# Performance work log

Hardware: AMD Instinct MI355X
Metric: run time of the kernel (lower is better)

Reference implementation:

```python
import jax, jax.numpy as jnp
import numpy as np

B, N, FH, H, FO = 8, 1024, 128, 8, 64
FIN = 2 * FH  # f_hid * 2
NEG = -1e9
SLOPE = 0.2  # leaky_relu negative slope (GAT default)


def setup_inputs() -> dict:
    key = jax.random.key(0)
    ks = jax.random.split(key, 10)
    x = jax.random.normal(ks[0], (B, FIN), jnp.float32)
    A = jax.random.randint(ks[1], (B, N, N), 0, 2, jnp.int32)  # 0/1 dense adjacency
    mask_zero = jnp.ones((B, N, 1), jnp.float32)  # node validity mask
    p_atten = jax.random.uniform(ks[2], (B, N), jnp.float32)  # unused in forward body
    e_atten = jax.random.uniform(ks[3], (B, N, FIN), jnp.float32)
    Npost = jax.random.normal(ks[4], (N, FIN), jnp.float32) * np.float32(1.0 / np.sqrt(FIN))  # kaiming-ish
    w = jax.random.normal(ks[5], (H, FIN, FO), jnp.float32) * np.float32(1.0 / np.sqrt(FIN))
    a_src = jax.random.normal(ks[6], (H, FO), jnp.float32) * np.float32(0.1)
    a_dst = jax.random.normal(ks[7], (H, FO), jnp.float32) * np.float32(0.1)
    bias = jnp.zeros((FO,), jnp.float32)
    return {"x": x, "A": A, "mask_zero": mask_zero, "p_atten": p_atten,
            "e_atten": e_atten, "Npost": Npost, "w": w, "a_src": a_src,
            "a_dst": a_dst, "bias": bias}


def reference(x, A, mask_zero, p_atten, e_atten, Npost, w, a_src, a_dst, bias):
    # broadcast-mul feature gating: x [B,FIN] repeated over N posts, gated by Npost*e_atten
    recx = x[:, None, :] * (Npost[None, :, :] * e_atten)          # [B,N,FIN]
    # BatchGAT (DeepInf-style multi-head graph attention, dropout disabled / eval mode)
    h = jnp.einsum('bnf,hfo->bhno', recx, w)                      # [B,H,N,FO]
    s = jnp.einsum('bhno,ho->bhn', h, a_src)                      # src attention term
    d = jnp.einsum('bhno,ho->bhn', h, a_dst)                      # dst attention term
    logits = jax.nn.leaky_relu(s[:, :, :, None] + d[:, :, None, :], SLOPE)  # [B,H,N,N]
    adj = (A > 0)[:, None, :, :]                                  # [B,1,N,N]
    logits = jnp.where(adj, logits, NEG)
    attn = jax.nn.softmax(logits, axis=-1)                        # masked row softmax
    out = jnp.einsum('bhnm,bhmo->bhno', attn, h) + bias           # aggregate neighbors
    out = out.mean(axis=1)                                        # average heads -> [B,N,FO]
    return out * mask_zero                                        # zero padded nodes
```

## Files before the change

kernel.cpp:

```cpp
#include <hip/hip_runtime.h>

typedef __attribute__((ext_vector_type(8))) short          bf16x8;
typedef __attribute__((ext_vector_type(8))) unsigned short u16x8;
typedef __attribute__((ext_vector_type(4))) unsigned short u16x4;
typedef __attribute__((ext_vector_type(4))) float          f32x4;
typedef __attribute__((ext_vector_type(4))) unsigned int   u32x4;

union U8 { u16x8 u; bf16x8 b; u32x4 w; };
union U4 { u16x4 u; unsigned w[2]; };

__device__ __forceinline__ unsigned short f2bf(float f){
  unsigned u = __float_as_uint(f);
  return (unsigned short)((u + 0x7fffu + ((u >> 16) & 1u)) >> 16);
}
__device__ __forceinline__ unsigned pack_bf16(float lo, float hi){
  unsigned a = __float_as_uint(hi) + 0x8000u;
  unsigned b = __float_as_uint(lo) + 0x8000u;
  return __builtin_amdgcn_perm(a, b, 0x07060302u);
}
__device__ __forceinline__ unsigned maskpack(float e0, float e1, unsigned m){
  unsigned r;
  asm("v_cvt_pk_bf16_f32 %0, %1, %2" : "=v"(r) : "v"(e0), "v"(e1));
  return r & m;
}

#define NN  1024
#define FIN 256
#define NH  8
#define FO  64

__global__ __launch_bounds__(256) void stage0(
    const float* __restrict__ w, unsigned short* __restrict__ wfrag)
{
  const int tid = blockIdx.x * 256 + threadIdx.x;
  const int lane = tid & 63, ss = (tid >> 6) & 3, kc = (tid >> 8) & 7, h = tid >> 11;
  const int o = 16 * ss + (lane & 15);
  const int f = kc * 32 + (lane >> 4) * 8;
  u16x8 r;
  #pragma unroll
  for (int j = 0; j < 8; j++) r[j] = f2bf(w[(h * FIN + f + j) * FO + o]);
  *(u16x8*)(wfrag + tid * 8) = r;
}

__global__ __launch_bounds__(512, 4) void stageA(
    const float* __restrict__ x, const float* __restrict__ e_at,
    const float* __restrict__ Np, const unsigned short* __restrict__ wfrag,
    const float* __restrict__ a_src, const float* __restrict__ a_dst,
    const int* __restrict__ A, unsigned long long* __restrict__ Abits,
    unsigned short* __restrict__ hT,
    float* __restrict__ Rt, float* __restrict__ expd, float* __restrict__ expd2)
{
  __shared__ unsigned short rex[16 * 264];
  const int t = threadIdx.x;
  const int n0 = blockIdx.x * 16, b = blockIdx.y;

  {
    const int row = t >> 5, f0 = (t & 31) * 8;
    const int nrow = n0 + row;
    const float* ep = e_at + (b * NN + nrow) * FIN + f0;
    const float* qp = Np + nrow * FIN + f0;
    const float* xp = x + b * FIN + f0;
    f32x4 e0 = *(const f32x4*)ep, e1 = *(const f32x4*)(ep + 4);
    f32x4 q0 = *(const f32x4*)qp, q1 = *(const f32x4*)(qp + 4);
    f32x4 x0 = *(const f32x4*)xp, x1 = *(const f32x4*)(xp + 4);
    u16x8 r;
    #pragma unroll
    for (int j = 0; j < 4; j++){
      r[j]     = f2bf(e0[j] * q0[j] * x0[j]);
      r[j + 4] = f2bf(e1[j] * q1[j] * x1[j]);
    }
    *(u16x8*)(rex + row * 264 + f0) = r;
  }
  __syncthreads();

  const int h = t >> 6, lane = t & 63, quad = lane >> 4, l15 = lane & 15;
  const unsigned short* wf = wfrag + h * 16384 + lane * 8;

  f32x4 acc[4] = {};
  #pragma unroll
  for (int kc = 0; kc < 8; kc++){
    U8 a0, bf[4];
    a0.u = *(const u16x8*)(rex + l15 * 264 + kc * 32 + quad * 8);
    #pragma unroll
    for (int ss = 0; ss < 4; ss++) bf[ss].u = *(const u16x8*)(wf + (kc * 4 + ss) * 512);
    #pragma unroll
    for (int ss = 0; ss < 4; ss++)
      acc[ss] = __builtin_amdgcn_mfma_f32_16x16x32_bf16(a0.b, bf[ss].b, acc[ss], 0, 0, 0);
  }

  {
    const int mtile = blockIdx.x >> 1, moff = (blockIdx.x & 1) * 16;
    unsigned short* pan = hT + (size_t)(((b * NH + h) * 32 + mtile) * 64) * 32;
    #pragma unroll
    for (int ss = 0; ss < 4; ss++){
      U4 v;
      v.w[0] = pack_bf16(acc[ss][0], acc[ss][1]);
      v.w[1] = pack_bf16(acc[ss][2], acc[ss][3]);
      *(u16x4*)(pan + (16 * ss + l15) * 32 + moff + quad * 4) = v.u;
    }
  }

  float as4[4], ad4[4];
  #pragma unroll
  for (int ss = 0; ss < 4; ss++){
    as4[ss] = a_src[h * FO + 16 * ss + l15];
    ad4[ss] = a_dst[h * FO + 16 * ss + l15];
  }
  #pragma unroll
  for (int i = 0; i < 4; i++){
    float ps = 0.f, pd = 0.f;
    #pragma unroll
    for (int ss = 0; ss < 4; ss++){ ps += acc[ss][i] * as4[ss]; pd += acc[ss][i] * ad4[ss]; }
    #pragma unroll
    for (int off = 1; off < 16; off <<= 1){
      ps += __shfl_xor(ps, off);
      pd += __shfl_xor(pd, off);
    }
    if (l15 == 0){
      const int idx = (b * NH + h) * NN + n0 + quad * 4 + i;
      Rt[idx]    = __expf(0.8f * ps);
      expd[idx]  = __expf(pd);
      expd2[idx] = __expf(0.2f * pd);
    }
  }

  {
    const int seg = (b * 64 + blockIdx.x) * 16384;
    #pragma unroll 4
    for (int k = 0; k < 32; k++){
      const int i = seg + k * 512 + t;
      unsigned long long m = __ballot(A[i] > 0);
      if ((t & 63) == 0) Abits[i >> 6] = m;
    }
  }
}

__global__ __launch_bounds__(256, 4) void stageB(
    const unsigned* __restrict__ Aw,
    const unsigned short* __restrict__ hT,
    const float* __restrict__ Rt,
    const float* __restrict__ expd, const float* __restrict__ expd2,
    float* __restrict__ hpart)
{
  __shared__ float smem[4288];
  __shared__ __align__(8) unsigned lut[16][2];

  const int fid = blockIdx.x;
  const int b = fid & 7, h = (fid >> 3) & 7, rt = fid >> 6;
  const int n0 = rt * 64;

  const int t = threadIdx.x;
  const int w = t >> 6, lane = t & 63, quad = lane >> 4, l15 = lane & 15;
  const int rw = w & 1, mh = w >> 1;
  const int nb = n0 + rw * 32;

  if (t < 16){
    lut[t][0] = (t & 1 ? 0xFFFFu : 0u) | (t & 2 ? 0xFFFF0000u : 0u);
    lut[t][1] = (t & 4 ? 0xFFFFu : 0u) | (t & 8 ? 0xFFFF0000u : 0u);
  }
  {
    const float* s1 = expd  + (b * NH + h) * NN;
    const float* s2 = expd2 + (b * NH + h) * NN;
    *(f32x4*)(smem + t * 4)        = *(const f32x4*)(s1 + t * 4);
    *(f32x4*)(smem + 1024 + t * 4) = *(const f32x4*)(s2 + t * 4);
  }
  __syncthreads();

  const int hb = (b * NH + h) * NN;
  const float Rv0 = Rt[hb + nb + l15];
  const float Rv1 = Rt[hb + nb + 16 + l15];
  const unsigned short* pb = hT + (size_t)(b * NH + h) * 65536 + l15 * 32 + quad * 8;
  const float* edh = smem + quad * 8;
  const float* e2h = smem + 1024 + quad * 8;
  const unsigned* awp = Aw + (b * NN + nb) * 32;
  const int c0 = mh * 16;
  const int qs = quad * 8;

  U8 panc[4], pann[4];
  #pragma unroll
  for (int ss = 0; ss < 4; ss++)
    panc[ss].u = *(const u16x8*)(pb + (size_t)c0 * 2048 + ss * 512);
  unsigned mwc0 = awp[l15 * 32 + c0];
  unsigned mwc1 = awp[(16 + l15) * 32 + c0];
  unsigned mwn0, mwn1;

  U8 ones;
  #pragma unroll
  for (int j = 0; j < 8; j++) ones.u[j] = 0x3F80;

  f32x4 acc0[4] = {}, acc1[4] = {};
  f32x4 accl0 = {}, accl1 = {};

  #pragma unroll
  for (int cc = 0; cc < 16; cc++){
    const int c = c0 + cc;
    if (cc + 1 < 16){
      #pragma unroll
      for (int ss = 0; ss < 4; ss++)
        pann[ss].u = *(const u16x8*)(pb + (size_t)(c + 1) * 2048 + ss * 512);
      mwn0 = awp[l15 * 32 + c + 1];
      mwn1 = awp[(16 + l15) * 32 + c + 1];
    }
    const unsigned am0 = (mwc0 >> qs) & 0xFF;
    const unsigned am1 = (mwc1 >> qs) & 0xFF;
    const uint2 la0 = *(const uint2*)&lut[am0 & 15][0];
    const uint2 lb0 = *(const uint2*)&lut[(am0 >> 4) & 15][0];
    const uint2 la1 = *(const uint2*)&lut[am1 & 15][0];
    const uint2 lb1 = *(const uint2*)&lut[(am1 >> 4) & 15][0];
    const f32x4 d01 = *(const f32x4*)(edh + c * 32);
    const f32x4 d23 = *(const f32x4*)(edh + c * 32 + 4);
    const f32x4 g01 = *(const f32x4*)(e2h + c * 32);
    const f32x4 g23 = *(const f32x4*)(e2h + c * 32 + 4);
    {
      const f32x4 p01 = Rv0 * d01, p23 = Rv0 * d23;
      U8 p;
      p.w[0] = maskpack(fmaxf(p01[0], g01[0]), fmaxf(p01[1], g01[1]), la0.x);
      p.w[1] = maskpack(fmaxf(p01[2], g01[2]), fmaxf(p01[3], g01[3]), la0.y);
      p.w[2] = maskpack(fmaxf(p23[0], g23[0]), fmaxf(p23[1], g23[1]), lb0.x);
      p.w[3] = maskpack(fmaxf(p23[2], g23[2]), fmaxf(p23[3], g23[3]), lb0.y);
      #pragma unroll
      for (int ss = 0; ss < 4; ss++)
        acc0[ss] = __builtin_amdgcn_mfma_f32_16x16x32_bf16(p.b, panc[ss].b, acc0[ss], 0, 0, 0);
      accl0 = __builtin_amdgcn_mfma_f32_16x16x32_bf16(p.b, ones.b, accl0, 0, 0, 0);
    }
    {
      const f32x4 p01 = Rv1 * d01, p23 = Rv1 * d23;
      U8 p;
      p.w[0] = maskpack(fmaxf(p01[0], g01[0]), fmaxf(p01[1], g01[1]), la1.x);
      p.w[1] = maskpack(fmaxf(p01[2], g01[2]), fmaxf(p01[3], g01[3]), la1.y);
      p.w[2] = maskpack(fmaxf(p23[0], g23[0]), fmaxf(p23[1], g23[1]), lb1.x);
      p.w[3] = maskpack(fmaxf(p23[2], g23[2]), fmaxf(p23[3], g23[3]), lb1.y);
      #pragma unroll
      for (int ss = 0; ss < 4; ss++)
        acc1[ss] = __builtin_amdgcn_mfma_f32_16x16x32_bf16(p.b, panc[ss].b, acc1[ss], 0, 0, 0);
      accl1 = __builtin_amdgcn_mfma_f32_16x16x32_bf16(p.b, ones.b, accl1, 0, 0, 0);
    }
    if (cc + 1 < 16){
      #pragma unroll
      for (int ss = 0; ss < 4; ss++) panc[ss] = pann[ss];
      mwc0 = mwn0; mwc1 = mwn1;
    }
  }

  __syncthreads();

  float* den = smem + 4160;
  if (l15 == 0){
    #pragma unroll
    for (int i = 0; i < 4; i++){
      den[mh * 64 + rw * 32 + quad * 4 + i]      = accl0[i];
      den[mh * 64 + rw * 32 + 16 + quad * 4 + i] = accl1[i];
    }
  }
  if (mh == 1){
    #pragma unroll
    for (int i = 0; i < 4; i++){
      const int r0 = rw * 32 + quad * 4 + i;
      #pragma unroll
      for (int ss = 0; ss < 4; ss++){
        smem[r0 * 65 + ss * 16 + l15]        = acc0[ss][i];
        smem[(r0 + 16) * 65 + ss * 16 + l15] = acc1[ss][i];
      }
    }
  }
  __syncthreads();

  if (mh == 0){
    float* hp = hpart + ((size_t)(b * NH + h) * NN + nb) * FO;
    #pragma unroll
    for (int i = 0; i < 4; i++){
      const int r = quad * 4 + i;
      const float ia = 1.0f / (den[rw * 32 + r] + den[64 + rw * 32 + r]);
      const float ib = 1.0f / (den[rw * 32 + 16 + r] + den[64 + rw * 32 + 16 + r]);
      #pragma unroll
      for (int ss = 0; ss < 4; ss++){
        hp[(size_t)r * FO + ss * 16 + l15] =
            (acc0[ss][i] + smem[(rw * 32 + r) * 65 + ss * 16 + l15]) * ia;
        hp[(size_t)(16 + r) * FO + ss * 16 + l15] =
            (acc1[ss][i] + smem[(rw * 32 + 16 + r) * 65 + ss * 16 + l15]) * ib;
      }
    }
  }
}

__global__ __launch_bounds__(256) void stageC(
    const float* __restrict__ hpart, const float* __restrict__ bias,
    const float* __restrict__ mz, float* __restrict__ out)
{
  const int tid = blockIdx.x * 256 + threadIdx.x;
  const int o4 = (tid & 15) * 4;
  const int n  = (tid >> 4) & 1023;
  const int b  = tid >> 14;
  const size_t nf = (size_t)n * FO + o4;
  f32x4 s = {};
  #pragma unroll
  for (int h = 0; h < NH; h++)
    s += *(const f32x4*)(hpart + (size_t)(b * NH + h) * NN * FO + nf);
  const f32x4 bv = *(const f32x4*)(bias + o4);
  const float m = mz[b * NN + n];
  f32x4 r;
  #pragma unroll
  for (int j = 0; j < 4; j++) r[j] = (0.125f * s[j] + bv[j]) * m;
  *(f32x4*)(out + (size_t)b * NN * FO + nf) = r;
}

extern "C" void kernel_launch(void* const* d_in, const int* in_sizes, int n_in,
                              void* d_out, int out_size, void* d_ws, size_t ws_size,
                              hipStream_t stream)
{
  (void)in_sizes; (void)n_in; (void)out_size; (void)ws_size;
  const float* x    = (const float*)d_in[0];
  const int*   A    = (const int*)d_in[1];
  const float* mz   = (const float*)d_in[2];
  const float* e_at = (const float*)d_in[4];
  const float* Np   = (const float*)d_in[5];
  const float* w    = (const float*)d_in[6];
  const float* asrc = (const float*)d_in[7];
  const float* adst = (const float*)d_in[8];
  const float* bias = (const float*)d_in[9];
  float* out = (float*)d_out;

  char* ws = (char*)d_ws;
  unsigned short* wfrag = (unsigned short*)ws;
  unsigned short* hT    = (unsigned short*)(ws + 262144);
  float* Rt    = (float*)(ws + 8650752);
  float* expd  = (float*)(ws + 8912896);
  float* expd2 = (float*)(ws + 9175040);
  unsigned long long* Abits = (unsigned long long*)(ws + 9437184);
  float* hpart = (float*)(ws + 10485760);

  stage0<<<dim3(64), dim3(256), 0, stream>>>(w, wfrag);
  stageA<<<dim3(64, 8), dim3(512), 0, stream>>>(x, e_at, Np, wfrag, asrc, adst,
                                                A, Abits, hT, Rt, expd, expd2);
  stageB<<<dim3(1024), dim3(256), 0, stream>>>((const unsigned*)Abits, hT,
                                               Rt, expd, expd2, hpart);
  stageC<<<dim3(512), dim3(256), 0, stream>>>(hpart, bias, mz, out);
}
```

Measured before the change: 151.3 us.

## Split attention K-dimension across four waves, each covering all 64 rows

The attention aggregation kernel now has each of its four waves cover all 64 query rows over one quarter of the neighbor chunks, instead of a 2x2 split of rows and neighbor halves. Each loaded hT fragment then feeds four row groups' MFMAs instead of two, cutting global loads per MFMA. The adjacency-to-mask shared-memory LUT is replaced by bit-field extract plus perm instructions. In exchange, register pressure rises (occupancy hint drops from 4 to 3 blocks), the explicit double-buffer prefetch is removed, and the cross-wave reduction needs more shared memory and extra barriers.

```diff
diff --git a/kernel.cpp b/kernel.cpp
--- a/kernel.cpp
+++ b/kernel.cpp
@@ -22,6 +22,11 @@
   unsigned r;
   asm("v_cvt_pk_bf16_f32 %0, %1, %2" : "=v"(r) : "v"(e0), "v"(e1));
   return r & m;
+}
+__device__ __forceinline__ unsigned bit2half(unsigned m, unsigned off){
+  unsigned lo = __builtin_amdgcn_sbfe((int)m, off, 1u);
+  unsigned hi = __builtin_amdgcn_sbfe((int)m, off + 1u, 1u);
+  return __builtin_amdgcn_perm(hi, lo, 0x05040100u);
 }
 
 #define NN  1024
@@ -135,15 +140,14 @@
   }
 }
 
-__global__ __launch_bounds__(256, 4) void stageB(
+__global__ __launch_bounds__(256, 3) void attnB(
     const unsigned* __restrict__ Aw,
     const unsigned short* __restrict__ hT,
     const float* __restrict__ Rt,
     const float* __restrict__ expd, const float* __restrict__ expd2,
     float* __restrict__ hpart)
 {
-  __shared__ float smem[4288];
-  __shared__ __align__(8) unsigned lut[16][2];
+  __shared__ float smem[8576];
 
   const int fid = blockIdx.x;
   const int b = fid & 7, h = (fid >> 3) & 7, rt = fid >> 6;
@@ -151,13 +155,8 @@
 
   const int t = threadIdx.x;
   const int w = t >> 6, lane = t & 63, quad = lane >> 4, l15 = lane & 15;
-  const int rw = w & 1, mh = w >> 1;
-  const int nb = n0 + rw * 32;
-
-  if (t < 16){
-    lut[t][0] = (t & 1 ? 0xFFFFu : 0u) | (t & 2 ? 0xFFFF0000u : 0u);
-    lut[t][1] = (t & 4 ? 0xFFFFu : 0u) | (t & 8 ? 0xFFFF0000u : 0u);
-  }
+  const int mh = w;
+
   {
     const float* s1 = expd  + (b * NH + h) * NN;
     const float* s2 = expd2 + (b * NH + h) * NN;
@@ -167,119 +166,127 @@
   __syncthreads();
 
   const int hb = (b * NH + h) * NN;
-  const float Rv0 = Rt[hb + nb + l15];
-  const float Rv1 = Rt[hb + nb + 16 + l15];
+  float Rv[4];
+  #pragma unroll
+  for (int g = 0; g < 4; g++) Rv[g] = Rt[hb + n0 + g * 16 + l15];
   const unsigned short* pb = hT + (size_t)(b * NH + h) * 65536 + l15 * 32 + quad * 8;
   const float* edh = smem + quad * 8;
   const float* e2h = smem + 1024 + quad * 8;
-  const unsigned* awp = Aw + (b * NN + nb) * 32;
-  const int c0 = mh * 16;
-  const int qs = quad * 8;
-
-  U8 panc[4], pann[4];
+  const unsigned* awp = Aw + (b * NN + n0) * 32;
+  const int c0 = mh * 8;
+  const unsigned qs = (unsigned)(quad * 8);
+
+  U8 pan[4];
   #pragma unroll
   for (int ss = 0; ss < 4; ss++)
-    panc[ss].u = *(const u16x8*)(pb + (size_t)c0 * 2048 + ss * 512);
-  unsigned mwc0 = awp[l15 * 32 + c0];
-  unsigned mwc1 = awp[(16 + l15) * 32 + c0];
-  unsigned mwn0, mwn1;
+    pan[ss].u = *(const u16x8*)(pb + (size_t)c0 * 2048 + ss * 512);
+  unsigned mw[4];
+  #pragma unroll
+  for (int g = 0; g < 4; g++) mw[g] = awp[(g * 16 + l15) * 32 + c0];
 
   U8 ones;
   #pragma unroll
   for (int j = 0; j < 8; j++) ones.u[j] = 0x3F80;
 
-  f32x4 acc0[4] = {}, acc1[4] = {};
-  f32x4 accl0 = {}, accl1 = {};
-
-  #pragma unroll
-  for (int cc = 0; cc < 16; cc++){
+  f32x4 acc[4][4] = {{}};
+  f32x4 accl[4] = {};
+
+  #pragma unroll
+  for (int cc = 0; cc < 8; cc++){
     const int c = c0 + cc;
-    if (cc + 1 < 16){
-      #pragma unroll
-      for (int ss = 0; ss < 4; ss++)
-        pann[ss].u = *(const u16x8*)(pb + (size_t)(c + 1) * 2048 + ss * 512);
-      mwn0 = awp[l15 * 32 + c + 1];
-      mwn1 = awp[(16 + l15) * 32 + c + 1];
-    }
-    const unsigned am0 = (mwc0 >> qs) & 0xFF;
-    const unsigned am1 = (mwc1 >> qs) & 0xFF;
-    const uint2 la0 = *(const uint2*)&lut[am0 & 15][0];
-    const uint2 lb0 = *(const uint2*)&lut[(am0 >> 4) & 15][0];
-    const uint2 la1 = *(const uint2*)&lut[am1 & 15][0];
-    const uint2 lb1 = *(const uint2*)&lut[(am1 >> 4) & 15][0];
     const f32x4 d01 = *(const f32x4*)(edh + c * 32);
     const f32x4 d23 = *(const f32x4*)(edh + c * 32 + 4);
     const f32x4 g01 = *(const f32x4*)(e2h + c * 32);
     const f32x4 g23 = *(const f32x4*)(e2h + c * 32 + 4);
-    {
-      const f32x4 p01 = Rv0 * d01, p23 = Rv0 * d23;
+    #pragma unroll
+    for (int g = 0; g < 4; g++){
+      const unsigned lax = bit2half(mw[g], qs + 0u), lay = bit2half(mw[g], qs + 2u);
+      const unsigned lbx = bit2half(mw[g], qs + 4u), lby = bit2half(mw[g], qs + 6u);
+      const f32x4 p01 = Rv[g] * d01, p23 = Rv[g] * d23;
       U8 p;
-      p.w[0] = maskpack(fmaxf(p01[0], g01[0]), fmaxf(p01[1], g01[1]), la0.x);
-      p.w[1] = maskpack(fmaxf(p01[2], g01[2]), fmaxf(p01[3], g01[3]), la0.y);
-      p.w[2] = maskpack(fmaxf(p23[0], g23[0]), fmaxf(p23[1], g23[1]), lb0.x);
-      p.w[3] = maskpack(fmaxf(p23[2], g23[2]), fmaxf(p23[3], g23[3]), lb0.y);
+      p.w[0] = maskpack(fmaxf(p01[0], g01[0]), fmaxf(p01[1], g01[1]), lax);
+      p.w[1] = maskpack(fmaxf(p01[2], g01[2]), fmaxf(p01[3], g01[3]), lay);
+      p.w[2] = maskpack(fmaxf(p23[0], g23[0]), fmaxf(p23[1], g23[1]), lbx);
+      p.w[3] = maskpack(fmaxf(p23[2], g23[2]), fmaxf(p23[3], g23[3]), lby);
       #pragma unroll
       for (int ss = 0; ss < 4; ss++)
-        acc0[ss] = __builtin_amdgcn_mfma_f32_16x16x32_bf16(p.b, panc[ss].b, acc0[ss], 0, 0, 0);
-      accl0 = __builtin_amdgcn_mfma_f32_16x16x32_bf16(p.b, ones.b, accl0, 0, 0, 0);
-    }
-    {
-      const f32x4 p01 = Rv1 * d01, p23 = Rv1 * d23;
-      U8 p;
-      p.w[0] = maskpack(fmaxf(p01[0], g01[0]), fmaxf(p01[1], g01[1]), la1.x);
-      p.w[1] = maskpack(fmaxf(p01[2], g01[2]), fmaxf(p01[3], g01[3]), la1.y);
-      p.w[2] = maskpack(fmaxf(p23[0], g23[0]), fmaxf(p23[1], g23[1]), lb1.x);
-      p.w[3] = maskpack(fmaxf(p23[2], g23[2]), fmaxf(p23[3], g23[3]), lb1.y);
+        acc[g][ss] = __builtin_amdgcn_mfma_f32_16x16x32_bf16(p.b, pan[ss].b, acc[g][ss], 0, 0, 0);
+      accl[g] = __builtin_amdgcn_mfma_f32_16x16x32_bf16(p.b, ones.b, accl[g], 0, 0, 0);
+    }
+    if (cc + 1 < 8){
+      #pragma unroll
+      for (int g = 0; g < 4; g++) mw[g] = awp[(g * 16 + l15) * 32 + c + 1];
       #pragma unroll
       for (int ss = 0; ss < 4; ss++)
-        acc1[ss] = __builtin_amdgcn_mfma_f32_16x16x32_bf16(p.b, panc[ss].b, acc1[ss], 0, 0, 0);
-      accl1 = __builtin_amdgcn_mfma_f32_16x16x32_bf16(p.b, ones.b, accl1, 0, 0, 0);
-    }
-    if (cc + 1 < 16){
-      #pragma unroll
-      for (int ss = 0; ss < 4; ss++) panc[ss] = pann[ss];
-      mwc0 = mwn0; mwc1 = mwn1;
-    }
-  }
-
-  __syncthreads();
-
-  float* den = smem + 4160;
+        pan[ss].u = *(const u16x8*)(pb + (size_t)(c + 1) * 2048 + ss * 512);
+    }
+  }
+
+  __syncthreads();
+
+  float* M0  = smem;
+  float* M1  = smem + 4160;
+  float* den = smem + 8320;
+
   if (l15 == 0){
     #pragma unroll
-    for (int i = 0; i < 4; i++){
-      den[mh * 64 + rw * 32 + quad * 4 + i]      = accl0[i];
-      den[mh * 64 + rw * 32 + 16 + quad * 4 + i] = accl1[i];
-    }
-  }
-  if (mh == 1){
-    #pragma unroll
-    for (int i = 0; i < 4; i++){
-      const int r0 = rw * 32 + quad * 4 + i;
-      #pragma unroll
-      for (int ss = 0; ss < 4; ss++){
-        smem[r0 * 65 + ss * 16 + l15]        = acc0[ss][i];
-        smem[(r0 + 16) * 65 + ss * 16 + l15] = acc1[ss][i];
+    for (int g = 0; g < 4; g++)
+      #pragma unroll
+      for (int i = 0; i < 4; i++)
+        den[mh * 64 + g * 16 + quad * 4 + i] = accl[g][i];
+  }
+  if (mh & 1){
+    float* M = (mh == 1) ? M0 : M1;
+    #pragma unroll
+    for (int g = 0; g < 4; g++)
+      #pragma unroll
+      for (int i = 0; i < 4; i++){
+        const int r = g * 16 + quad * 4 + i;
+        #pragma unroll
+        for (int ss = 0; ss < 4; ss++)
+          M[r * 65 + ss * 16 + l15] = acc[g][ss][i];
       }
-    }
-  }
-  __syncthreads();
-
+  }
+  __syncthreads();
+  if (mh == 0 || mh == 2){
+    const float* M = (mh == 0) ? M0 : M1;
+    #pragma unroll
+    for (int g = 0; g < 4; g++)
+      #pragma unroll
+      for (int i = 0; i < 4; i++){
+        const int r = g * 16 + quad * 4 + i;
+        #pragma unroll
+        for (int ss = 0; ss < 4; ss++)
+          acc[g][ss][i] += M[r * 65 + ss * 16 + l15];
+      }
+  }
+  __syncthreads();
+  if (mh == 2){
+    #pragma unroll
+    for (int g = 0; g < 4; g++)
+      #pragma unroll
+      for (int i = 0; i < 4; i++){
+        const int r = g * 16 + quad * 4 + i;
+        #pragma unroll
+        for (int ss = 0; ss < 4; ss++)
+          M0[r * 65 + ss * 16 + l15] = acc[g][ss][i];
+      }
+  }
+  __syncthreads();
   if (mh == 0){
-    float* hp = hpart + ((size_t)(b * NH + h) * NN + nb) * FO;
-    #pragma unroll
-    for (int i = 0; i < 4; i++){
-      const int r = quad * 4 + i;
-      const float ia = 1.0f / (den[rw * 32 + r] + den[64 + rw * 32 + r]);
-      const float ib = 1.0f / (den[rw * 32 + 16 + r] + den[64 + rw * 32 + 16 + r]);
-      #pragma unroll
-      for (int ss = 0; ss < 4; ss++){
-        hp[(size_t)r * FO + ss * 16 + l15] =
-            (acc0[ss][i] + smem[(rw * 32 + r) * 65 + ss * 16 + l15]) * ia;
-        hp[(size_t)(16 + r) * FO + ss * 16 + l15] =
-            (acc1[ss][i] + smem[(rw * 32 + 16 + r) * 65 + ss * 16 + l15]) * ib;
+    float* hp = hpart + ((size_t)(b * NH + h) * NN + n0) * FO;
+    #pragma unroll
+    for (int g = 0; g < 4; g++)
+      #pragma unroll
+      for (int i = 0; i < 4; i++){
+        const int r = g * 16 + quad * 4 + i;
+        const float inv = 1.0f /
+            (den[r] + den[64 + r] + den[128 + r] + den[192 + r]);
+        #pragma unroll
+        for (int ss = 0; ss < 4; ss++)
+          hp[(size_t)r * FO + ss * 16 + l15] =
+              (acc[g][ss][i] + M0[r * 65 + ss * 16 + l15]) * inv;
       }
-    }
   }
 }
 
@@ -332,7 +339,7 @@
   stage0<<<dim3(64), dim3(256), 0, stream>>>(w, wfrag);
   stageA<<<dim3(64, 8), dim3(512), 0, stream>>>(x, e_at, Np, wfrag, asrc, adst,
                                                 A, Abits, hT, Rt, expd, expd2);
-  stageB<<<dim3(1024), dim3(256), 0, stream>>>((const unsigned*)Abits, hT,
-                                               Rt, expd, expd2, hpart);
+  attnB<<<dim3(1024), dim3(256), 0, stream>>>((const unsigned*)Abits, hT,
+                                              Rt, expd, expd2, hpart);
   stageC<<<dim3(512), dim3(256), 0, stream>>>(hpart, bias, mz, out);
 }
```

New measurement: 177.5 us. 1.17x slower.
